# Kernel optimization log

Measured on AMD Instinct MI355X. Metric: run time of the kernel, lower is better.

## Reference

```python
import jax, jax.numpy as jnp
import numpy as np
import math

A, R, E, H = 4, 2, 12, 24  # msg_angular, msg_radial, embed_dim, hidden_dim
N = A * R
B, L = 131072, 15

def _ring_adj(n):
    adj = np.zeros((n, n), np.float32)
    if n == 1:
        adj[0, 0] = 1.0
    else:
        for i in range(n):
            adj[i, (i - 1) % n] = 1.0
            adj[i, (i + 1) % n] = 1.0
    return jnp.asarray(adj)

ANG_ADJ = _ring_adj(A)
RAD_ADJ = _ring_adj(R)

def setup_inputs():
    key = jax.random.key(0)
    ks = jax.random.split(key, 16)
    p = lambda k, s: jax.random.normal(k, s, jnp.float32) * 0.1
    return {
        "x": jax.random.normal(ks[0], (B, L, 4), jnp.float32),
        "enc_w1": p(ks[1], (4, H)), "enc_b1": p(ks[2], (H,)),
        "enc_w2": p(ks[3], (H, H)), "enc_b2": p(ks[4], (H,)),
        "enc_w3": p(ks[5], (H, 3)), "enc_b3": p(ks[6], (3,)),
        "node_w1": p(ks[7], (E, H)), "node_b1": p(ks[8], (H,)),
        "node_w2": p(ks[9], (H, E)), "node_b2": p(ks[10], (E,)),
        "angular_logit": jnp.zeros((A,), jnp.float32),
        "radial_logit": jnp.zeros((R,), jnp.float32),
        "read_w1": p(ks[11], (E * N, H)), "read_b1": p(ks[12], (H,)),
        "read_w2": p(ks[13], (H, 4)), "read_b2": p(ks[14], (4,)),
    }

def _norm_adj(logit, adj):
    a = jax.nn.softmax(logit)[None, :] * adj
    return a / jnp.maximum(a.sum(1, keepdims=True), 1e-6)

def _forward(x, enc_w1, enc_b1, enc_w2, enc_b2, enc_w3, enc_b3,
             node_w1, node_b1, node_w2, node_b2,
             angular_logit, radial_logit,
             read_w1, read_b1, read_w2, read_b2):
    b = x.shape[0]
    # encoder: original loops over all timesteps but only uses the last z
    zt = jnp.tanh(x[:, -1, :] @ enc_w1 + enc_b1)
    zt = jnp.tanh(zt @ enc_w2 + enc_b2)
    z = zt @ enc_w3 + enc_b3                       # [B, 3]
    r = jax.nn.sigmoid(z[:, 0]) * (R - 1)          # R_idx in [0, R-1]
    p = (z[:, 1] + math.pi) / (2 * math.pi) * A    # phi_idx (can be <0 or >A)
    # torch code calls .item(), detaching indices/weights from autograd
    r = jax.lax.stop_gradient(r)
    p = jax.lax.stop_gradient(p)
    r0 = jnp.trunc(r)   # int() truncates toward zero
    p0 = jnp.trunc(p)
    dr = (r - r0)[:, None]
    dp = (p - p0)[:, None]
    dro = jnp.array([0.0, 0.0, 1.0, 1.0], jnp.float32)   # 4 bilinear corners
    dpo = jnp.array([0.0, 1.0, 0.0, 1.0], jnp.float32)
    wr = jnp.where(dro == 0, 1.0 - dr, dr)               # [B, 4]
    wp = jnp.where(dpo == 0, 1.0 - dp, dp)
    w = wr * wp                                          # [B, 4]
    r_i = jnp.minimum(r0.astype(jnp.int32)[:, None] + dro.astype(jnp.int32), R - 1)
    p_i = jnp.mod(p0.astype(jnp.int32)[:, None] + dpo.astype(jnp.int32), A)
    mask = (w > 0).astype(x.dtype)[:, :, None]           # 'if weight > 0' skip
    # node_embed = pad(concat([z, weight]), E); z entries are NOT weight-scaled
    vec = jnp.concatenate([
        jnp.broadcast_to(z[:, None, :], (b, 4, 3)),
        w[:, :, None],
        jnp.zeros((b, 4, E - 4), x.dtype)], axis=-1) * mask   # [B, 4, E]
    grid = jnp.zeros((b, R, A, E), x.dtype).at[
        jnp.arange(b)[:, None], r_i, p_i].add(vec)            # scatter-add
    h = grid.reshape(b, N, E)
    ang = _norm_adj(angular_logit, ANG_ADJ)  # [A, A]
    rad = _norm_adj(radial_logit, RAD_ADJ)   # [R, R]
    # faithful to the torch .view() layout mixing (r,a,e)
    h_ang = jnp.einsum('ij,bjk->bik', ang, h.reshape(b, A, R * E)).reshape(b, N, E)
    h_rad = jnp.einsum('ij,bjk->bik', rad, h.reshape(b, R, A * E)).reshape(b, N, E)
    h = h + h_ang + h_rad
    h = jnp.tanh(h @ node_w1 + node_b1) @ node_w2 + node_b2   # node_net
    out = jnp.tanh(h.reshape(b, -1) @ read_w1 + read_b1) @ read_w2 + read_b2
    return out  # [B, 4]

def reference(x, enc_w1, enc_b1, enc_w2, enc_b2, enc_w3, enc_b3,
              node_w1, node_b1, node_w2, node_b2,
              angular_logit, radial_logit,
              read_w1, read_b1, read_w2, read_b2):
    return _forward(x, enc_w1, enc_b1, enc_w2, enc_b2, enc_w3, enc_b3,
                    node_w1, node_b1, node_w2, node_b2,
                    angular_logit, radial_logit,
                    read_w1, read_b1, read_w2, read_b2)
```

## Files before the change

kernel.cpp:

```cpp
#include <hip/hip_runtime.h>
#include <math.h>


#define PI_F 3.14159265358979323846f

typedef float f32x2 __attribute__((ext_vector_type(2)));

__device__ __forceinline__ f32x2 b2(float v) { f32x2 r; r.x = v; r.y = v; return r; }
__device__ __forceinline__ f32x2 pkfma(f32x2 a, f32x2 b, f32x2 c) {
    return __builtin_elementwise_fma(a, b, c);
}

__device__ __forceinline__ float fast_tanh(float v) {
    float e = __expf(2.0f * v);
    return 1.0f - 2.0f * __builtin_amdgcn_rcpf(e + 1.0f);
}

__device__ __forceinline__ f32x2 tanh2(f32x2 v) {
    f32x2 e; e.x = __expf(2.0f * v.x); e.y = __expf(2.0f * v.y);
    f32x2 ep = e + b2(1.0f);
    f32x2 r; r.x = __builtin_amdgcn_rcpf(ep.x); r.y = __builtin_amdgcn_rcpf(ep.y);
    return pkfma(b2(-2.0f), r, b2(1.0f));
}

__device__ __forceinline__ float quad_sum(float x) {
    x += __int_as_float(__builtin_amdgcn_update_dpp(
             0, __float_as_int(x), 0xB1, 0xF, 0xF, true));
    x += __int_as_float(__builtin_amdgcn_update_dpp(
             0, __float_as_int(x), 0x4E, 0xF, 0xF, true));
    return x;
}

__device__ __forceinline__ float xor4_sum(float x) {
    return x + __int_as_float(
        __builtin_amdgcn_ds_swizzle(__float_as_int(x), 0x101F));
}

#define K1_LDS 880

extern "C" __global__ void __launch_bounds__(256, 2)
topo_k1(const float* __restrict__ x,
        const float* __restrict__ ew1, const float* __restrict__ eb1,
        const float* __restrict__ ew2, const float* __restrict__ eb2,
        const float* __restrict__ ew3, const float* __restrict__ eb3,
        const float* __restrict__ alog, const float* __restrict__ rlog,
        const float* __restrict__ nw2, const float* __restrict__ nb2,
        const float* __restrict__ rw1, const float* __restrict__ rb1,
        float* __restrict__ ws, int B)
{
    const int nb1b = (B + 255) >> 8;

    if ((int)blockIdx.x >= nb1b) {
        const int gid = ((int)blockIdx.x - nb1b) * 256 + (int)threadIdx.x;
        float* M = ws + (size_t)B * 20;
        if (gid < 4608) {
            const int cell = gid / 576, rem = gid - cell * 576;
            const int j = rem / 24, j2 = rem - j * 24;
            double s = 0.0;
            #pragma unroll
            for (int d = 0; d < 12; ++d)
                s += (double)nw2[j * 12 + d] * (double)rw1[(cell * 12 + d) * 24 + j2];
            M[gid] = (float)s;
        } else if (gid < 4632) {
            const int j2 = gid - 4608;
            double s = (double)rb1[j2];
            for (int i = 0; i < 96; ++i)
                s += (double)nb2[i % 12] * (double)rw1[i * 24 + j2];
            M[4608 + j2] = (float)s;
        }
        return;
    }

    __shared__ float wf[K1_LDS];
    const float4* wq = reinterpret_cast<const float4*>(wf);
    {
        const int tt = threadIdx.x;
        for (int i = tt; i < 24; i += 256) {
            wf[i * 8 + 0] = ew1[i];
            wf[i * 8 + 1] = ew1[24 + i];
            wf[i * 8 + 2] = ew1[48 + i];
            wf[i * 8 + 3] = ew1[72 + i];
            wf[i * 8 + 4] = eb1[i];
        }
        for (int i = tt; i < 576; i += 256) wf[192 + i] = ew2[i];
        for (int i = tt; i < 24;  i += 256) wf[768 + i] = eb2[i];
        for (int i = tt; i < 72;  i += 256) wf[792 + (i % 3) * 24 + (i / 3)] = ew3[i];
        for (int i = tt; i < 3;   i += 256) wf[864 + i] = eb3[i];
    }
    __syncthreads();

    const int b = blockIdx.x * blockDim.x + threadIdx.x;
    if (b >= B) return;

    const float4 xv = *reinterpret_cast<const float4*>(x + (size_t)b * 60 + 56);

    f32x2 A2[12];
    #pragma unroll
    for (int c = 0; c < 6; ++c) {
        float4 b4 = wq[192 / 4 + c];
        A2[c*2+0].x = b4.x; A2[c*2+0].y = b4.y;
        A2[c*2+1].x = b4.z; A2[c*2+1].y = b4.w;
    }
    #pragma unroll 2
    for (int k = 0; k < 24; ++k) {
        float4 p  = wq[2 * k];
        float4 p2 = wq[2 * k + 1];
        const float zk = fast_tanh(p2.x + xv.x*p.x + xv.y*p.y + xv.z*p.z + xv.w*p.w);
        const f32x2 zk2 = b2(zk);
        const int rr = 48 + k * 6;
        #pragma unroll
        for (int c = 0; c < 6; ++c) {
            float4 rv = wq[rr + c];
            f32x2 r01; r01.x = rv.x; r01.y = rv.y;
            f32x2 r23; r23.x = rv.z; r23.y = rv.w;
            A2[c*2+0] = pkfma(zk2, r01, A2[c*2+0]);
            A2[c*2+1] = pkfma(zk2, r23, A2[c*2+1]);
        }
    }
    float zt2[24];
    #pragma unroll
    for (int j = 0; j < 24; ++j)
        zt2[j] = fast_tanh((j & 1) ? A2[j >> 1].y : A2[j >> 1].x);

    float z0 = wf[864], z1 = wf[865], z2 = wf[866];
    #pragma unroll
    for (int c = 0; c < 6; ++c) {
        float4 v0 = wq[198 + c], v1 = wq[204 + c], v2 = wq[210 + c];
        z0 += zt2[c*4+0]*v0.x + zt2[c*4+1]*v0.y + zt2[c*4+2]*v0.z + zt2[c*4+3]*v0.w;
        z1 += zt2[c*4+0]*v1.x + zt2[c*4+1]*v1.y + zt2[c*4+2]*v1.z + zt2[c*4+3]*v1.w;
        z2 += zt2[c*4+0]*v2.x + zt2[c*4+1]*v2.y + zt2[c*4+2]*v2.z + zt2[c*4+3]*v2.w;
    }

    float ang[4][4];
    {
        float m = fmaxf(fmaxf(alog[0], alog[1]), fmaxf(alog[2], alog[3]));
        float e0 = __expf(alog[0] - m), e1 = __expf(alog[1] - m);
        float e2 = __expf(alog[2] - m), e3 = __expf(alog[3] - m);
        float s = e0 + e1 + e2 + e3;
        float sm[4] = { e0 / s, e1 / s, e2 / s, e3 / s };
        #pragma unroll
        for (int i = 0; i < 4; ++i) {
            const int jn = (i + 3) & 3, jp = (i + 1) & 3;
            float inv = 1.0f / fmaxf(sm[jn] + sm[jp], 1e-6f);
            #pragma unroll
            for (int j = 0; j < 4; ++j) {
                float adj = (j == jn || j == jp) ? 1.0f : 0.0f;
                ang[i][j] = sm[j] * adj * inv;
            }
        }
    }
    float rad[2][2];
    {
        float m = fmaxf(rlog[0], rlog[1]);
        float f0 = __expf(rlog[0] - m), f1 = __expf(rlog[1] - m);
        float fs = f0 + f1;
        float sm0 = f0 / fs, sm1 = f1 / fs;
        rad[0][0] = 0.0f; rad[0][1] = sm1 / fmaxf(sm1, 1e-6f);
        rad[1][1] = 0.0f; rad[1][0] = sm0 / fmaxf(sm0, 1e-6f);
    }

    const float r = 1.0f / (1.0f + __expf(-z0));
    const float p = (z1 + PI_F) / (2.0f * PI_F) * 4.0f;
    const float r0f = truncf(r), p0f = truncf(p);
    const float dr = r - r0f, dp = p - p0f;
    const int r0i = (int)r0f, p0i = (int)p0f;

    const float w0c = (1.0f - dr) * (1.0f - dp);
    const float w1c = (1.0f - dr) * dp;
    const float w2c = dr * (1.0f - dp);
    const float w3c = dr * dp;

    const int ri0 = min(r0i, 1);
    const int ri2 = min(r0i + 1, 1);
    const int pi0 = p0i & 3;
    const int pi1 = (p0i + 1) & 3;

    const int c0 = ri0 * 4 + pi0, c1 = ri0 * 4 + pi1;
    const int c2 = ri2 * 4 + pi0, c3 = ri2 * 4 + pi1;

    float cnt[8], wsum[8];
    #pragma unroll
    for (int n = 0; n < 8; ++n) {
        float cm = 0.0f, cw = 0.0f;
        if (c0 == n && w0c > 0.0f) { cm += 1.0f; cw += w0c; }
        if (c1 == n && w1c > 0.0f) { cm += 1.0f; cw += w1c; }
        if (c2 == n && w2c > 0.0f) { cm += 1.0f; cw += w2c; }
        if (c3 == n && w3c > 0.0f) { cm += 1.0f; cw += w3c; }
        cnt[n] = cm; wsum[n] = cw;
    }
    float mc[8], mw[8];
    #pragma unroll
    for (int n = 0; n < 8; ++n) {
        float ac = cnt[n], aw = wsum[n];
        #pragma unroll
        for (int j = 0; j < 4; ++j) {
            const float g = ang[n >> 1][j];
            ac += g * cnt[2 * j + (n & 1)];
            aw += g * wsum[2 * j + (n & 1)];
        }
        #pragma unroll
        for (int j = 0; j < 2; ++j) {
            const float g = rad[n >> 2][j];
            ac += g * cnt[4 * j + (n & 3)];
            aw += g * wsum[4 * j + (n & 3)];
        }
        mc[n] = ac; mw[n] = aw;
    }

    float* wp = ws + (size_t)b * 20;
    float4 v0; v0.x = z0;    v0.y = z1;    v0.z = z2;    v0.w = 0.0f;
    float4 v1; v1.x = mc[0]; v1.y = mc[1]; v1.z = mc[2]; v1.w = mc[3];
    float4 v2; v2.x = mc[4]; v2.y = mc[5]; v2.z = mc[6]; v2.w = mc[7];
    float4 v3; v3.x = mw[0]; v3.y = mw[1]; v3.z = mw[2]; v3.w = mw[3];
    float4 v4; v4.x = mw[4]; v4.y = mw[5]; v4.z = mw[6]; v4.w = mw[7];
    reinterpret_cast<float4*>(wp)[0] = v0;
    reinterpret_cast<float4*>(wp)[1] = v1;
    reinterpret_cast<float4*>(wp)[2] = v2;
    reinterpret_cast<float4*>(wp)[3] = v3;
    reinterpret_cast<float4*>(wp)[4] = v4;
}

#define K2_LDS 4956

extern "C" __global__ void __launch_bounds__(256)
topo_k2(const float* __restrict__ ws,
        const float* __restrict__ nw1, const float* __restrict__ nb1,
        const float* __restrict__ rw2, const float* __restrict__ rb2,
        float* __restrict__ out, int B)
{
    __shared__ float wf[K2_LDS];
    const float4* wq = reinterpret_cast<const float4*>(wf);
    {
        const int tt = threadIdx.x;
        const float* Msrc = ws + (size_t)B * 20;
        for (int i = tt; i < 4608; i += 256) {
            const int cell = i / 576, rem = i - cell * 576;
            wf[192 + cell * 580 + rem] = Msrc[i];
        }
        for (int i = tt; i < 24; i += 256) wf[4832 + i] = Msrc[4608 + i];
        for (int i = tt; i < 24; i += 256) {
            wf[i * 8 + 0] = nw1[i];
            wf[i * 8 + 1] = nw1[24 + i];
            wf[i * 8 + 2] = nw1[48 + i];
            wf[i * 8 + 3] = nw1[72 + i];
            wf[i * 8 + 4] = nb1[i];
        }
        for (int i = tt; i < 96; i += 256) wf[4856 + i] = rw2[i];
        for (int i = tt; i < 4;  i += 256) wf[4952 + i] = rb2[i];
    }
    __syncthreads();

    const int tid  = blockIdx.x * blockDim.x + threadIdx.x;
    const int cp   = tid & 3;
    const int half = (tid >> 2) & 1;
    const int slot = tid >> 3;
    const int nP   = (B + 1) >> 1;
    if (slot >= nP) return;
    const int e0  = 2 * slot;
    const int e1s = 2 * slot + 1;
    const int e1  = (e1s < B) ? e1s : (B - 1);

    const float* wp0 = ws + (size_t)e0 * 20;
    const float* wp1 = ws + (size_t)e1 * 20;
    const float4 zA4 = *reinterpret_cast<const float4*>(wp0);
    const float4 zB4 = *reinterpret_cast<const float4*>(wp1);
    const float2 mc0 = *reinterpret_cast<const float2*>(wp0 + 4 + 2 * cp);
    const float2 mw0 = *reinterpret_cast<const float2*>(wp0 + 12 + 2 * cp);
    const float2 mc1 = *reinterpret_cast<const float2*>(wp1 + 4 + 2 * cp);
    const float2 mw1 = *reinterpret_cast<const float2*>(wp1 + 12 + 2 * cp);

    f32x2 ZX; ZX.x = zA4.x; ZX.y = zB4.x;
    f32x2 ZY; ZY.x = zA4.y; ZY.y = zB4.y;
    f32x2 ZZ; ZZ.x = zA4.z; ZZ.y = zB4.z;
    f32x2 MCA; MCA.x = mc0.x; MCA.y = mc1.x;
    f32x2 MCB; MCB.x = mc0.y; MCB.y = mc1.y;
    f32x2 MWA; MWA.x = mw0.x; MWA.y = mw1.x;
    f32x2 MWB; MWB.x = mw0.y; MWB.y = mw1.y;

    const int mA = 48 + (2 * cp) * 145 + half * 3;
    const int mB = mA + 145;

    f32x2 T0[6], T1[6];
    #pragma unroll
    for (int k = 0; k < 6; ++k) { T0[k] = b2(0.0f); T1[k] = b2(0.0f); }

    #pragma unroll 1
    for (int j = 0; j < 24; ++j) {
        float4 pk  = wq[2 * j];
        float4 pk2 = wq[2 * j + 1];
        f32x2 Q = ZX * b2(pk.x);
        Q = pkfma(ZY, b2(pk.y), Q);
        Q = pkfma(ZZ, b2(pk.z), Q);
        f32x2 baseA = pkfma(MWA, b2(pk.w), b2(pk2.x));
        f32x2 baseB = pkfma(MWB, b2(pk.w), b2(pk2.x));
        f32x2 HA = tanh2(pkfma(MCA, Q, baseA));
        f32x2 HB = tanh2(pkfma(MCB, Q, baseB));

        const int ra = mA + j * 6, rb = mB + j * 6;
        float4 a0 = wq[ra], a1 = wq[ra + 1], a2v = wq[ra + 2];
        float4 bb0 = wq[rb], bb1 = wq[rb + 1], bb2 = wq[rb + 2];
        f32x2 A0; A0.x = a0.x;  A0.y = a0.y;
        f32x2 A1; A1.x = a0.z;  A1.y = a0.w;
        f32x2 A2; A2.x = a1.x;  A2.y = a1.y;
        f32x2 A3; A3.x = a1.z;  A3.y = a1.w;
        f32x2 A4; A4.x = a2v.x; A4.y = a2v.y;
        f32x2 A5; A5.x = a2v.z; A5.y = a2v.w;
        f32x2 B0; B0.x = bb0.x; B0.y = bb0.y;
        f32x2 B1; B1.x = bb0.z; B1.y = bb0.w;
        f32x2 B2; B2.x = bb1.x; B2.y = bb1.y;
        f32x2 B3; B3.x = bb1.z; B3.y = bb1.w;
        f32x2 B4; B4.x = bb2.x; B4.y = bb2.y;
        f32x2 B5; B5.x = bb2.z; B5.y = bb2.w;

        const f32x2 hA0 = b2(HA.x), hA1 = b2(HA.y);
        const f32x2 hB0 = b2(HB.x), hB1 = b2(HB.y);
        T0[0] = pkfma(hA0, A0, T0[0]); T0[1] = pkfma(hA0, A1, T0[1]);
        T0[2] = pkfma(hA0, A2, T0[2]); T0[3] = pkfma(hA0, A3, T0[3]);
        T0[4] = pkfma(hA0, A4, T0[4]); T0[5] = pkfma(hA0, A5, T0[5]);
        T1[0] = pkfma(hA1, A0, T1[0]); T1[1] = pkfma(hA1, A1, T1[1]);
        T1[2] = pkfma(hA1, A2, T1[2]); T1[3] = pkfma(hA1, A3, T1[3]);
        T1[4] = pkfma(hA1, A4, T1[4]); T1[5] = pkfma(hA1, A5, T1[5]);
        T0[0] = pkfma(hB0, B0, T0[0]); T0[1] = pkfma(hB0, B1, T0[1]);
        T0[2] = pkfma(hB0, B2, T0[2]); T0[3] = pkfma(hB0, B3, T0[3]);
        T0[4] = pkfma(hB0, B4, T0[4]); T0[5] = pkfma(hB0, B5, T0[5]);
        T1[0] = pkfma(hB1, B0, T1[0]); T1[1] = pkfma(hB1, B1, T1[1]);
        T1[2] = pkfma(hB1, B2, T1[2]); T1[3] = pkfma(hB1, B3, T1[3]);
        T1[4] = pkfma(hB1, B4, T1[4]); T1[5] = pkfma(hB1, B5, T1[5]);
    }

    float t0[12], t1[12];
    #pragma unroll
    for (int k = 0; k < 12; ++k) {
        t0[k] = (k & 1) ? T0[k >> 1].y : T0[k >> 1].x;
        t1[k] = (k & 1) ? T1[k >> 1].y : T1[k >> 1].x;
    }

    #pragma unroll
    for (int k = 0; k < 12; ++k) {
        t0[k] = quad_sum(t0[k]);
        t1[k] = quad_sum(t1[k]);
    }
    #pragma unroll
    for (int c = 0; c < 3; ++c) {
        float4 ti = wq[1208 + half * 3 + c];
        t0[c*4+0] += ti.x; t0[c*4+1] += ti.y; t0[c*4+2] += ti.z; t0[c*4+3] += ti.w;
        t1[c*4+0] += ti.x; t1[c*4+1] += ti.y; t1[c*4+2] += ti.z; t1[c*4+3] += ti.w;
    }

    float o00 = 0.0f, o01 = 0.0f, o02 = 0.0f, o03 = 0.0f;
    float o10 = 0.0f, o11 = 0.0f, o12 = 0.0f, o13 = 0.0f;
    #pragma unroll
    for (int k = 0; k < 12; ++k) {
        const float tv0 = fast_tanh(t0[k]);
        const float tv1 = fast_tanh(t1[k]);
        float4 rv = wq[1214 + half * 12 + k];
        o00 += tv0 * rv.x; o01 += tv0 * rv.y; o02 += tv0 * rv.z; o03 += tv0 * rv.w;
        o10 += tv1 * rv.x; o11 += tv1 * rv.y; o12 += tv1 * rv.z; o13 += tv1 * rv.w;
    }
    o00 = xor4_sum(o00); o01 = xor4_sum(o01); o02 = xor4_sum(o02); o03 = xor4_sum(o03);
    o10 = xor4_sum(o10); o11 = xor4_sum(o11); o12 = xor4_sum(o12); o13 = xor4_sum(o13);

    if ((tid & 7) == 0) {
        float4 ob = wq[1238];
        float4 ovA; ovA.x = o00 + ob.x; ovA.y = o01 + ob.y;
        ovA.z = o02 + ob.z; ovA.w = o03 + ob.w;
        *reinterpret_cast<float4*>(out + (size_t)e0 * 4) = ovA;
        if (e1s < B) {
            float4 ovB; ovB.x = o10 + ob.x; ovB.y = o11 + ob.y;
            ovB.z = o12 + ob.z; ovB.w = o13 + ob.w;
            *reinterpret_cast<float4*>(out + (size_t)e1s * 4) = ovB;
        }
    }
}

extern "C" __global__ void __launch_bounds__(256, 2)
topo_fused(const float* __restrict__ x,
           const float* __restrict__ ew1, const float* __restrict__ eb1,
           const float* __restrict__ ew2, const float* __restrict__ eb2,
           const float* __restrict__ ew3, const float* __restrict__ eb3,
           const float* __restrict__ nw1, const float* __restrict__ nb1,
           const float* __restrict__ nw2, const float* __restrict__ nb2,
           const float* __restrict__ alog, const float* __restrict__ rlog,
           const float* __restrict__ rw1, const float* __restrict__ rb1,
           const float* __restrict__ rw2, const float* __restrict__ rb2,
           float* __restrict__ out, int B)
{
    const int b = blockIdx.x * blockDim.x + threadIdx.x;
    if (b >= B) return;

    float ang[4][4];
    {
        float m = fmaxf(fmaxf(alog[0], alog[1]), fmaxf(alog[2], alog[3]));
        float e0 = __expf(alog[0] - m), e1 = __expf(alog[1] - m);
        float e2 = __expf(alog[2] - m), e3 = __expf(alog[3] - m);
        float s = e0 + e1 + e2 + e3;
        float sm[4] = { e0 / s, e1 / s, e2 / s, e3 / s };
        #pragma unroll
        for (int i = 0; i < 4; ++i) {
            const int jn = (i + 3) & 3, jp = (i + 1) & 3;
            float inv = 1.0f / fmaxf(sm[jn] + sm[jp], 1e-6f);
            #pragma unroll
            for (int j = 0; j < 4; ++j) {
                float adj = (j == jn || j == jp) ? 1.0f : 0.0f;
                ang[i][j] = sm[j] * adj * inv;
            }
        }
    }
    float rad[2][2];
    {
        float m = fmaxf(rlog[0], rlog[1]);
        float f0 = __expf(rlog[0] - m), f1 = __expf(rlog[1] - m);
        float fs = f0 + f1;
        float sm0 = f0 / fs, sm1 = f1 / fs;
        rad[0][0] = 0.0f; rad[0][1] = sm1 / fmaxf(sm1, 1e-6f);
        rad[1][1] = 0.0f; rad[1][0] = sm0 / fmaxf(sm0, 1e-6f);
    }

    const float4 xv = *reinterpret_cast<const float4*>(x + (size_t)b * 60 + 56);
    float zt[24];
    #pragma unroll
    for (int j = 0; j < 24; ++j) {
        float a = eb1[j];
        a += xv.x * ew1[j];
        a += xv.y * ew1[24 + j];
        a += xv.z * ew1[48 + j];
        a += xv.w * ew1[72 + j];
        zt[j] = fast_tanh(a);
    }
    float z0 = eb3[0], z1 = eb3[1], z2 = eb3[2];
    #pragma unroll
    for (int j = 0; j < 24; ++j) {
        float a = eb2[j];
        #pragma unroll
        for (int k = 0; k < 24; ++k) a += zt[k] * ew2[k * 24 + j];
        const float z2t = fast_tanh(a);
        z0 += z2t * ew3[j * 3 + 0];
        z1 += z2t * ew3[j * 3 + 1];
        z2 += z2t * ew3[j * 3 + 2];
    }

    const float r = 1.0f / (1.0f + __expf(-z0));
    const float p = (z1 + PI_F) / (2.0f * PI_F) * 4.0f;
    const float r0f = truncf(r), p0f = truncf(p);
    const float dr = r - r0f, dp = p - p0f;
    const int r0i = (int)r0f, p0i = (int)p0f;
    const float w0c = (1.0f - dr) * (1.0f - dp);
    const float w1c = (1.0f - dr) * dp;
    const float w2c = dr * (1.0f - dp);
    const float w3c = dr * dp;
    const int ri0 = min(r0i, 1);
    const int ri2 = min(r0i + 1, 1);
    const int pi0 = p0i & 3;
    const int pi1 = (p0i + 1) & 3;
    const int c0 = ri0 * 4 + pi0, c1 = ri0 * 4 + pi1;
    const int c2 = ri2 * 4 + pi0, c3 = ri2 * 4 + pi1;

    float cnt[8], wsum[8];
    #pragma unroll
    for (int n = 0; n < 8; ++n) {
        float cm = 0.0f, cw = 0.0f;
        if (c0 == n && w0c > 0.0f) { cm += 1.0f; cw += w0c; }
        if (c1 == n && w1c > 0.0f) { cm += 1.0f; cw += w1c; }
        if (c2 == n && w2c > 0.0f) { cm += 1.0f; cw += w2c; }
        if (c3 == n && w3c > 0.0f) { cm += 1.0f; cw += w3c; }
        cnt[n] = cm; wsum[n] = cw;
    }
    float mc[8], mw[8];
    #pragma unroll
    for (int n = 0; n < 8; ++n) {
        float ac = cnt[n], aw = wsum[n];
        #pragma unroll
        for (int j = 0; j < 4; ++j) {
            const float g = ang[n >> 1][j];
            ac += g * cnt[2 * j + (n & 1)];
            aw += g * wsum[2 * j + (n & 1)];
        }
        #pragma unroll
        for (int j = 0; j < 2; ++j) {
            const float g = rad[n >> 2][j];
            ac += g * cnt[4 * j + (n & 3)];
            aw += g * wsum[4 * j + (n & 3)];
        }
        mc[n] = ac; mw[n] = aw;
    }

    float t[24];
    #pragma unroll
    for (int j = 0; j < 24; ++j) t[j] = rb1[j];
    #pragma unroll
    for (int n = 0; n < 8; ++n) {
        const float f0 = mc[n] * z0, f1 = mc[n] * z1, f2 = mc[n] * z2;
        float ho[12];
        #pragma unroll
        for (int d = 0; d < 12; ++d) ho[d] = nb2[d];
        #pragma unroll
        for (int j = 0; j < 24; ++j) {
            const float hj = fast_tanh(nb1[j] + f0 * nw1[j] + f1 * nw1[24 + j]
                                       + f2 * nw1[48 + j] + mw[n] * nw1[72 + j]);
            #pragma unroll
            for (int d = 0; d < 12; ++d) ho[d] += hj * nw2[j * 12 + d];
        }
        #pragma unroll
        for (int d = 0; d < 12; ++d) {
            const int rbase = (n * 12 + d) * 24;
            #pragma unroll
            for (int j2 = 0; j2 < 24; ++j2) t[j2] += ho[d] * rw1[rbase + j2];
        }
    }

    float o0 = rb2[0], o1 = rb2[1], o2 = rb2[2], o3 = rb2[3];
    #pragma unroll
    for (int j = 0; j < 24; ++j) {
        const float tt = fast_tanh(t[j]);
        o0 += tt * rw2[j * 4 + 0];
        o1 += tt * rw2[j * 4 + 1];
        o2 += tt * rw2[j * 4 + 2];
        o3 += tt * rw2[j * 4 + 3];
    }
    float4 ov; ov.x = o0; ov.y = o1; ov.z = o2; ov.w = o3;
    *reinterpret_cast<float4*>(out + (size_t)b * 4) = ov;
}

extern "C" void kernel_launch(void* const* d_in, const int* in_sizes, int n_in,
                              void* d_out, int out_size, void* d_ws, size_t ws_size,
                              hipStream_t stream) {
    const float* x    = (const float*)d_in[0];
    const float* ew1  = (const float*)d_in[1];
    const float* eb1  = (const float*)d_in[2];
    const float* ew2  = (const float*)d_in[3];
    const float* eb2  = (const float*)d_in[4];
    const float* ew3  = (const float*)d_in[5];
    const float* eb3  = (const float*)d_in[6];
    const float* nw1  = (const float*)d_in[7];
    const float* nb1  = (const float*)d_in[8];
    const float* nw2  = (const float*)d_in[9];
    const float* nb2  = (const float*)d_in[10];
    const float* alog = (const float*)d_in[11];
    const float* rlog = (const float*)d_in[12];
    const float* rw1  = (const float*)d_in[13];
    const float* rb1  = (const float*)d_in[14];
    const float* rw2  = (const float*)d_in[15];
    const float* rb2  = (const float*)d_in[16];
    float* out = (float*)d_out;

    const int B = in_sizes[0] / 60;
    const size_t ws_needed = ((size_t)B * 20 + 4632) * sizeof(float);

    if (ws_size >= ws_needed) {
        float* ws = (float*)d_ws;
        const int nb1b = (B + 255) / 256;
        const int g1 = nb1b + 19;
        topo_k1<<<g1, 256, 0, stream>>>(x, ew1, eb1, ew2, eb2, ew3, eb3,
                                        alog, rlog, nw2, nb2, rw1, rb1, ws, B);
        const long long nP = ((long long)B + 1) / 2;
        const long long tot2 = nP * 8;
        const int g2 = (int)((tot2 + 255) / 256);
        topo_k2<<<g2, 256, 0, stream>>>(ws, nw1, nb1, rw2, rb2, out, B);
    } else {
        const int g = (B + 255) / 256;
        topo_fused<<<g, 256, 0, stream>>>(
            x, ew1, eb1, ew2, eb2, ew3, eb3, nw1, nb1, nw2, nb2,
            alog, rlog, rw1, rb1, rw2, rb2, out, B);
    }
}
```

Baseline: 50.21 us.

## Fuse encoder and readout kernels into one block-per-64-samples kernel

Replaces the two-kernel pipeline, which passed per-sample features through a global workspace, with one fused kernel. Each block handles 64 samples: half the threads run the encoder with two threads per sample (pair reduction through DPP), while the other half compute the folded node_w2·read_w1 matrix into LDS. The readout stage then runs from LDS in the same block. This removes the workspace round trip and one kernel launch, but every block now recomputes the 4632-entry folded weight matrix in float instead of double, adding redundant per-block work and using more LDS.

```diff
diff --git a/kernel.cpp b/kernel.cpp
--- a/kernel.cpp
+++ b/kernel.cpp
@@ -7,6 +7,7 @@
 typedef float f32x2 __attribute__((ext_vector_type(2)));
 
 __device__ __forceinline__ f32x2 b2(float v) { f32x2 r; r.x = v; r.y = v; return r; }
+__device__ __forceinline__ f32x2 mk2(float a, float b) { f32x2 r; r.x = a; r.y = b; return r; }
 __device__ __forceinline__ f32x2 pkfma(f32x2 a, f32x2 b, f32x2 c) {
     return __builtin_elementwise_fma(a, b, c);
 }
@@ -21,6 +22,12 @@
     f32x2 ep = e + b2(1.0f);
     f32x2 r; r.x = __builtin_amdgcn_rcpf(ep.x); r.y = __builtin_amdgcn_rcpf(ep.y);
     return pkfma(b2(-2.0f), r, b2(1.0f));
+}
+
+__device__ __forceinline__ float pair_sum(float x) {
+    x += __int_as_float(__builtin_amdgcn_update_dpp(
+             0, __float_as_int(x), 0xB1, 0xF, 0xF, true));
+    return x;
 }
 
 __device__ __forceinline__ float quad_sum(float x) {
@@ -36,45 +43,25 @@
         __builtin_amdgcn_ds_swizzle(__float_as_int(x), 0x101F));
 }
 
-#define K1_LDS 880
+#define FUSED_LDS 7116
 
 extern "C" __global__ void __launch_bounds__(256, 2)
-topo_k1(const float* __restrict__ x,
-        const float* __restrict__ ew1, const float* __restrict__ eb1,
-        const float* __restrict__ ew2, const float* __restrict__ eb2,
-        const float* __restrict__ ew3, const float* __restrict__ eb3,
-        const float* __restrict__ alog, const float* __restrict__ rlog,
-        const float* __restrict__ nw2, const float* __restrict__ nb2,
-        const float* __restrict__ rw1, const float* __restrict__ rb1,
-        float* __restrict__ ws, int B)
+topo_fused64(const float* __restrict__ x,
+             const float* __restrict__ ew1, const float* __restrict__ eb1,
+             const float* __restrict__ ew2, const float* __restrict__ eb2,
+             const float* __restrict__ ew3, const float* __restrict__ eb3,
+             const float* __restrict__ nw1, const float* __restrict__ nb1,
+             const float* __restrict__ nw2, const float* __restrict__ nb2,
+             const float* __restrict__ alog, const float* __restrict__ rlog,
+             const float* __restrict__ rw1, const float* __restrict__ rb1,
+             const float* __restrict__ rw2, const float* __restrict__ rb2,
+             float* __restrict__ out, int B)
 {
-    const int nb1b = (B + 255) >> 8;
-
-    if ((int)blockIdx.x >= nb1b) {
-        const int gid = ((int)blockIdx.x - nb1b) * 256 + (int)threadIdx.x;
-        float* M = ws + (size_t)B * 20;
-        if (gid < 4608) {
-            const int cell = gid / 576, rem = gid - cell * 576;
-            const int j = rem / 24, j2 = rem - j * 24;
-            double s = 0.0;
-            #pragma unroll
-            for (int d = 0; d < 12; ++d)
-                s += (double)nw2[j * 12 + d] * (double)rw1[(cell * 12 + d) * 24 + j2];
-            M[gid] = (float)s;
-        } else if (gid < 4632) {
-            const int j2 = gid - 4608;
-            double s = (double)rb1[j2];
-            for (int i = 0; i < 96; ++i)
-                s += (double)nb2[i % 12] * (double)rw1[i * 24 + j2];
-            M[4608 + j2] = (float)s;
-        }
-        return;
-    }
-
-    __shared__ float wf[K1_LDS];
+    __shared__ float wf[FUSED_LDS];
     const float4* wq = reinterpret_cast<const float4*>(wf);
+    const int tt = threadIdx.x;
+
     {
-        const int tt = threadIdx.x;
         for (int i = tt; i < 24; i += 256) {
             wf[i * 8 + 0] = ew1[i];
             wf[i * 8 + 1] = ew1[24 + i];
@@ -86,198 +73,196 @@
         for (int i = tt; i < 24;  i += 256) wf[768 + i] = eb2[i];
         for (int i = tt; i < 72;  i += 256) wf[792 + (i % 3) * 24 + (i / 3)] = ew3[i];
         for (int i = tt; i < 3;   i += 256) wf[864 + i] = eb3[i];
+        for (int i = tt; i < 24;  i += 256) {
+            wf[880 + i * 8 + 0] = nw1[i];
+            wf[880 + i * 8 + 1] = nw1[24 + i];
+            wf[880 + i * 8 + 2] = nw1[48 + i];
+            wf[880 + i * 8 + 3] = nw1[72 + i];
+            wf[880 + i * 8 + 4] = nb1[i];
+        }
+        for (int i = tt; i < 96; i += 256) wf[5736 + i] = rw2[i];
+        for (int i = tt; i < 4;  i += 256) wf[5832 + i] = rb2[i];
     }
     __syncthreads();
 
-    const int b = blockIdx.x * blockDim.x + threadIdx.x;
-    if (b >= B) return;
-
-    const float4 xv = *reinterpret_cast<const float4*>(x + (size_t)b * 60 + 56);
-
-    f32x2 A2[12];
-    #pragma unroll
-    for (int c = 0; c < 6; ++c) {
-        float4 b4 = wq[192 / 4 + c];
-        A2[c*2+0].x = b4.x; A2[c*2+0].y = b4.y;
-        A2[c*2+1].x = b4.z; A2[c*2+1].y = b4.w;
-    }
-    #pragma unroll 2
-    for (int k = 0; k < 24; ++k) {
-        float4 p  = wq[2 * k];
-        float4 p2 = wq[2 * k + 1];
-        const float zk = fast_tanh(p2.x + xv.x*p.x + xv.y*p.y + xv.z*p.z + xv.w*p.w);
-        const f32x2 zk2 = b2(zk);
-        const int rr = 48 + k * 6;
-        #pragma unroll
-        for (int c = 0; c < 6; ++c) {
-            float4 rv = wq[rr + c];
-            f32x2 r01; r01.x = rv.x; r01.y = rv.y;
-            f32x2 r23; r23.x = rv.z; r23.y = rv.w;
-            A2[c*2+0] = pkfma(zk2, r01, A2[c*2+0]);
-            A2[c*2+1] = pkfma(zk2, r23, A2[c*2+1]);
-        }
-    }
-    float zt2[24];
-    #pragma unroll
-    for (int j = 0; j < 24; ++j)
-        zt2[j] = fast_tanh((j & 1) ? A2[j >> 1].y : A2[j >> 1].x);
-
-    float z0 = wf[864], z1 = wf[865], z2 = wf[866];
-    #pragma unroll
-    for (int c = 0; c < 6; ++c) {
-        float4 v0 = wq[198 + c], v1 = wq[204 + c], v2 = wq[210 + c];
-        z0 += zt2[c*4+0]*v0.x + zt2[c*4+1]*v0.y + zt2[c*4+2]*v0.z + zt2[c*4+3]*v0.w;
-        z1 += zt2[c*4+0]*v1.x + zt2[c*4+1]*v1.y + zt2[c*4+2]*v1.z + zt2[c*4+3]*v1.w;
-        z2 += zt2[c*4+0]*v2.x + zt2[c*4+1]*v2.y + zt2[c*4+2]*v2.z + zt2[c*4+3]*v2.w;
-    }
-
-    float ang[4][4];
-    {
-        float m = fmaxf(fmaxf(alog[0], alog[1]), fmaxf(alog[2], alog[3]));
-        float e0 = __expf(alog[0] - m), e1 = __expf(alog[1] - m);
-        float e2 = __expf(alog[2] - m), e3 = __expf(alog[3] - m);
-        float s = e0 + e1 + e2 + e3;
-        float sm[4] = { e0 / s, e1 / s, e2 / s, e3 / s };
-        #pragma unroll
-        for (int i = 0; i < 4; ++i) {
-            const int jn = (i + 3) & 3, jp = (i + 1) & 3;
-            float inv = 1.0f / fmaxf(sm[jn] + sm[jp], 1e-6f);
+    const int base = blockIdx.x * 64;
+
+    if (tt < 128) {
+        const int el = tt >> 1;
+        const int h  = tt & 1;
+        const int b  = base + el;
+
+        const float4 xv = *reinterpret_cast<const float4*>(x + (size_t)b * 60 + 56);
+
+        float a2h[12];
+        #pragma unroll
+        for (int c = 0; c < 3; ++c) {
+            float4 b4 = wq[192 + 3 * h + c];
+            a2h[c*4+0] = b4.x; a2h[c*4+1] = b4.y;
+            a2h[c*4+2] = b4.z; a2h[c*4+3] = b4.w;
+        }
+        #pragma unroll 2
+        for (int k = 0; k < 24; ++k) {
+            float4 p  = wq[2 * k];
+            float4 p2 = wq[2 * k + 1];
+            const float zk = fast_tanh(p2.x + xv.x*p.x + xv.y*p.y + xv.z*p.z + xv.w*p.w);
+            #pragma unroll
+            for (int c = 0; c < 3; ++c) {
+                float4 rv = wq[48 + 6 * k + 3 * h + c];
+                a2h[c*4+0] += zk * rv.x; a2h[c*4+1] += zk * rv.y;
+                a2h[c*4+2] += zk * rv.z; a2h[c*4+3] += zk * rv.w;
+            }
+        }
+        float zt2h[12];
+        #pragma unroll
+        for (int j = 0; j < 12; ++j) zt2h[j] = fast_tanh(a2h[j]);
+
+        float z0p = 0.0f, z1p = 0.0f, z2p = 0.0f;
+        #pragma unroll
+        for (int c = 0; c < 3; ++c) {
+            float4 v0 = wq[198 + 3 * h + c];
+            float4 v1 = wq[204 + 3 * h + c];
+            float4 v2 = wq[210 + 3 * h + c];
+            z0p += zt2h[c*4+0]*v0.x + zt2h[c*4+1]*v0.y + zt2h[c*4+2]*v0.z + zt2h[c*4+3]*v0.w;
+            z1p += zt2h[c*4+0]*v1.x + zt2h[c*4+1]*v1.y + zt2h[c*4+2]*v1.z + zt2h[c*4+3]*v1.w;
+            z2p += zt2h[c*4+0]*v2.x + zt2h[c*4+1]*v2.y + zt2h[c*4+2]*v2.z + zt2h[c*4+3]*v2.w;
+        }
+        const float z0 = pair_sum(z0p) + wf[864];
+        const float z1 = pair_sum(z1p) + wf[865];
+        const float z2 = pair_sum(z2p) + wf[866];
+
+        float ang[4][4];
+        {
+            float m = fmaxf(fmaxf(alog[0], alog[1]), fmaxf(alog[2], alog[3]));
+            float e0 = __expf(alog[0] - m), e1 = __expf(alog[1] - m);
+            float e2 = __expf(alog[2] - m), e3 = __expf(alog[3] - m);
+            float s = e0 + e1 + e2 + e3;
+            float sm[4] = { e0 / s, e1 / s, e2 / s, e3 / s };
+            #pragma unroll
+            for (int i = 0; i < 4; ++i) {
+                const int jn = (i + 3) & 3, jp = (i + 1) & 3;
+                float inv = 1.0f / fmaxf(sm[jn] + sm[jp], 1e-6f);
+                #pragma unroll
+                for (int j = 0; j < 4; ++j) {
+                    float adj = (j == jn || j == jp) ? 1.0f : 0.0f;
+                    ang[i][j] = sm[j] * adj * inv;
+                }
+            }
+        }
+        float rad[2][2];
+        {
+            float m = fmaxf(rlog[0], rlog[1]);
+            float f0 = __expf(rlog[0] - m), f1 = __expf(rlog[1] - m);
+            float fs = f0 + f1;
+            float sm0 = f0 / fs, sm1 = f1 / fs;
+            rad[0][0] = 0.0f; rad[0][1] = sm1 / fmaxf(sm1, 1e-6f);
+            rad[1][1] = 0.0f; rad[1][0] = sm0 / fmaxf(sm0, 1e-6f);
+        }
+
+        const float r = 1.0f / (1.0f + __expf(-z0));
+        const float p = (z1 + PI_F) / (2.0f * PI_F) * 4.0f;
+        const float r0f = truncf(r), p0f = truncf(p);
+        const float dr = r - r0f, dp = p - p0f;
+        const int r0i = (int)r0f, p0i = (int)p0f;
+
+        const float w0c = (1.0f - dr) * (1.0f - dp);
+        const float w1c = (1.0f - dr) * dp;
+        const float w2c = dr * (1.0f - dp);
+        const float w3c = dr * dp;
+
+        const int ri0 = min(r0i, 1);
+        const int ri2 = min(r0i + 1, 1);
+        const int pi0 = p0i & 3;
+        const int pi1 = (p0i + 1) & 3;
+
+        const int c0 = ri0 * 4 + pi0, c1 = ri0 * 4 + pi1;
+        const int c2 = ri2 * 4 + pi0, c3 = ri2 * 4 + pi1;
+
+        float cnt[8], wsum[8];
+        #pragma unroll
+        for (int n = 0; n < 8; ++n) {
+            float cm = 0.0f, cw = 0.0f;
+            if (c0 == n && w0c > 0.0f) { cm += 1.0f; cw += w0c; }
+            if (c1 == n && w1c > 0.0f) { cm += 1.0f; cw += w1c; }
+            if (c2 == n && w2c > 0.0f) { cm += 1.0f; cw += w2c; }
+            if (c3 == n && w3c > 0.0f) { cm += 1.0f; cw += w3c; }
+            cnt[n] = cm; wsum[n] = cw;
+        }
+        float mc[8], mw[8];
+        #pragma unroll
+        for (int n = 0; n < 8; ++n) {
+            float ac = cnt[n], aw = wsum[n];
             #pragma unroll
             for (int j = 0; j < 4; ++j) {
-                float adj = (j == jn || j == jp) ? 1.0f : 0.0f;
-                ang[i][j] = sm[j] * adj * inv;
+                const float g = ang[n >> 1][j];
+                ac += g * cnt[2 * j + (n & 1)];
+                aw += g * wsum[2 * j + (n & 1)];
             }
-        }
-    }
-    float rad[2][2];
-    {
-        float m = fmaxf(rlog[0], rlog[1]);
-        float f0 = __expf(rlog[0] - m), f1 = __expf(rlog[1] - m);
-        float fs = f0 + f1;
-        float sm0 = f0 / fs, sm1 = f1 / fs;
-        rad[0][0] = 0.0f; rad[0][1] = sm1 / fmaxf(sm1, 1e-6f);
-        rad[1][1] = 0.0f; rad[1][0] = sm0 / fmaxf(sm0, 1e-6f);
-    }
-
-    const float r = 1.0f / (1.0f + __expf(-z0));
-    const float p = (z1 + PI_F) / (2.0f * PI_F) * 4.0f;
-    const float r0f = truncf(r), p0f = truncf(p);
-    const float dr = r - r0f, dp = p - p0f;
-    const int r0i = (int)r0f, p0i = (int)p0f;
-
-    const float w0c = (1.0f - dr) * (1.0f - dp);
-    const float w1c = (1.0f - dr) * dp;
-    const float w2c = dr * (1.0f - dp);
-    const float w3c = dr * dp;
-
-    const int ri0 = min(r0i, 1);
-    const int ri2 = min(r0i + 1, 1);
-    const int pi0 = p0i & 3;
-    const int pi1 = (p0i + 1) & 3;
-
-    const int c0 = ri0 * 4 + pi0, c1 = ri0 * 4 + pi1;
-    const int c2 = ri2 * 4 + pi0, c3 = ri2 * 4 + pi1;
-
-    float cnt[8], wsum[8];
-    #pragma unroll
-    for (int n = 0; n < 8; ++n) {
-        float cm = 0.0f, cw = 0.0f;
-        if (c0 == n && w0c > 0.0f) { cm += 1.0f; cw += w0c; }
-        if (c1 == n && w1c > 0.0f) { cm += 1.0f; cw += w1c; }
-        if (c2 == n && w2c > 0.0f) { cm += 1.0f; cw += w2c; }
-        if (c3 == n && w3c > 0.0f) { cm += 1.0f; cw += w3c; }
-        cnt[n] = cm; wsum[n] = cw;
-    }
-    float mc[8], mw[8];
-    #pragma unroll
-    for (int n = 0; n < 8; ++n) {
-        float ac = cnt[n], aw = wsum[n];
-        #pragma unroll
-        for (int j = 0; j < 4; ++j) {
-            const float g = ang[n >> 1][j];
-            ac += g * cnt[2 * j + (n & 1)];
-            aw += g * wsum[2 * j + (n & 1)];
-        }
-        #pragma unroll
-        for (int j = 0; j < 2; ++j) {
-            const float g = rad[n >> 2][j];
-            ac += g * cnt[4 * j + (n & 3)];
-            aw += g * wsum[4 * j + (n & 3)];
-        }
-        mc[n] = ac; mw[n] = aw;
-    }
-
-    float* wp = ws + (size_t)b * 20;
-    float4 v0; v0.x = z0;    v0.y = z1;    v0.z = z2;    v0.w = 0.0f;
-    float4 v1; v1.x = mc[0]; v1.y = mc[1]; v1.z = mc[2]; v1.w = mc[3];
-    float4 v2; v2.x = mc[4]; v2.y = mc[5]; v2.z = mc[6]; v2.w = mc[7];
-    float4 v3; v3.x = mw[0]; v3.y = mw[1]; v3.z = mw[2]; v3.w = mw[3];
-    float4 v4; v4.x = mw[4]; v4.y = mw[5]; v4.z = mw[6]; v4.w = mw[7];
-    reinterpret_cast<float4*>(wp)[0] = v0;
-    reinterpret_cast<float4*>(wp)[1] = v1;
-    reinterpret_cast<float4*>(wp)[2] = v2;
-    reinterpret_cast<float4*>(wp)[3] = v3;
-    reinterpret_cast<float4*>(wp)[4] = v4;
-}
-
-#define K2_LDS 4956
-
-extern "C" __global__ void __launch_bounds__(256)
-topo_k2(const float* __restrict__ ws,
-        const float* __restrict__ nw1, const float* __restrict__ nb1,
-        const float* __restrict__ rw2, const float* __restrict__ rb2,
-        float* __restrict__ out, int B)
-{
-    __shared__ float wf[K2_LDS];
-    const float4* wq = reinterpret_cast<const float4*>(wf);
-    {
-        const int tt = threadIdx.x;
-        const float* Msrc = ws + (size_t)B * 20;
-        for (int i = tt; i < 4608; i += 256) {
+            #pragma unroll
+            for (int j = 0; j < 2; ++j) {
+                const float g = rad[n >> 2][j];
+                ac += g * cnt[4 * j + (n & 3)];
+                aw += g * wsum[4 * j + (n & 3)];
+            }
+            mc[n] = ac; mw[n] = aw;
+        }
+
+        if (h == 0) {
+            float4* sp = reinterpret_cast<float4*>(&wf[5836 + 20 * el]);
+            float4 v0; v0.x = z0;    v0.y = z1;    v0.z = z2;    v0.w = 0.0f;
+            float4 v1; v1.x = mc[0]; v1.y = mc[1]; v1.z = mc[2]; v1.w = mc[3];
+            float4 v2; v2.x = mc[4]; v2.y = mc[5]; v2.z = mc[6]; v2.w = mc[7];
+            float4 v3; v3.x = mw[0]; v3.y = mw[1]; v3.z = mw[2]; v3.w = mw[3];
+            float4 v4; v4.x = mw[4]; v4.y = mw[5]; v4.z = mw[6]; v4.w = mw[7];
+            sp[0] = v0; sp[1] = v1; sp[2] = v2; sp[3] = v3; sp[4] = v4;
+        }
+    } else {
+        const int w = tt - 128;
+        #pragma unroll 1
+        for (int t = 0; t < 36; ++t) {
+            const int i = w + 128 * t;
             const int cell = i / 576, rem = i - cell * 576;
-            wf[192 + cell * 580 + rem] = Msrc[i];
-        }
-        for (int i = tt; i < 24; i += 256) wf[4832 + i] = Msrc[4608 + i];
-        for (int i = tt; i < 24; i += 256) {
-            wf[i * 8 + 0] = nw1[i];
-            wf[i * 8 + 1] = nw1[24 + i];
-            wf[i * 8 + 2] = nw1[48 + i];
-            wf[i * 8 + 3] = nw1[72 + i];
-            wf[i * 8 + 4] = nb1[i];
-        }
-        for (int i = tt; i < 96; i += 256) wf[4856 + i] = rw2[i];
-        for (int i = tt; i < 4;  i += 256) wf[4952 + i] = rb2[i];
+            const int j = rem / 24, j2 = rem - j * 24;
+            float s = 0.0f;
+            #pragma unroll
+            for (int d = 0; d < 12; ++d)
+                s += nw2[j * 12 + d] * rw1[(cell * 12 + d) * 24 + j2];
+            wf[1072 + cell * 580 + rem] = s;
+        }
+        if (w < 24) {
+            float s = rb1[w];
+            #pragma unroll 1
+            for (int i = 0; i < 96; ++i)
+                s += nb2[i % 12] * rw1[i * 24 + w];
+            wf[5712 + w] = s;
+        }
     }
     __syncthreads();
 
-    const int tid  = blockIdx.x * blockDim.x + threadIdx.x;
-    const int cp   = tid & 3;
-    const int half = (tid >> 2) & 1;
-    const int slot = tid >> 3;
-    const int nP   = (B + 1) >> 1;
-    if (slot >= nP) return;
-    const int e0  = 2 * slot;
-    const int e1s = 2 * slot + 1;
-    const int e1  = (e1s < B) ? e1s : (B - 1);
-
-    const float* wp0 = ws + (size_t)e0 * 20;
-    const float* wp1 = ws + (size_t)e1 * 20;
-    const float4 zA4 = *reinterpret_cast<const float4*>(wp0);
-    const float4 zB4 = *reinterpret_cast<const float4*>(wp1);
-    const float2 mc0 = *reinterpret_cast<const float2*>(wp0 + 4 + 2 * cp);
-    const float2 mw0 = *reinterpret_cast<const float2*>(wp0 + 12 + 2 * cp);
-    const float2 mc1 = *reinterpret_cast<const float2*>(wp1 + 4 + 2 * cp);
-    const float2 mw1 = *reinterpret_cast<const float2*>(wp1 + 12 + 2 * cp);
-
-    f32x2 ZX; ZX.x = zA4.x; ZX.y = zB4.x;
-    f32x2 ZY; ZY.x = zA4.y; ZY.y = zB4.y;
-    f32x2 ZZ; ZZ.x = zA4.z; ZZ.y = zB4.z;
-    f32x2 MCA; MCA.x = mc0.x; MCA.y = mc1.x;
-    f32x2 MCB; MCB.x = mc0.y; MCB.y = mc1.y;
-    f32x2 MWA; MWA.x = mw0.x; MWA.y = mw1.x;
-    f32x2 MWB; MWB.x = mw0.y; MWB.y = mw1.y;
-
-    const int mA = 48 + (2 * cp) * 145 + half * 3;
+    const int cp   = tt & 3;
+    const int half = (tt >> 2) & 1;
+    const int slot = tt >> 3;
+    const int eL0  = 2 * slot;
+    const int eL1  = 2 * slot + 1;
+
+    const float* sp0 = &wf[5836 + 20 * eL0];
+    const float* sp1 = &wf[5836 + 20 * eL1];
+    const float4 zA4 = *reinterpret_cast<const float4*>(sp0);
+    const float4 zB4 = *reinterpret_cast<const float4*>(sp1);
+    const float2 mc0 = *reinterpret_cast<const float2*>(sp0 + 4 + 2 * cp);
+    const float2 mw0 = *reinterpret_cast<const float2*>(sp0 + 12 + 2 * cp);
+    const float2 mc1 = *reinterpret_cast<const float2*>(sp1 + 4 + 2 * cp);
+    const float2 mw1 = *reinterpret_cast<const float2*>(sp1 + 12 + 2 * cp);
+
+    const f32x2 ZX = mk2(zA4.x, zB4.x);
+    const f32x2 ZY = mk2(zA4.y, zB4.y);
+    const f32x2 ZZ = mk2(zA4.z, zB4.z);
+    const f32x2 MCA = mk2(mc0.x, mc1.x);
+    const f32x2 MCB = mk2(mc0.y, mc1.y);
+    const f32x2 MWA = mk2(mw0.x, mw1.x);
+    const f32x2 MWB = mk2(mw0.y, mw1.y);
+
+    const int mA = 268 + (2 * cp) * 145 + half * 3;
     const int mB = mA + 145;
 
     f32x2 T0[6], T1[6];
@@ -286,8 +271,8 @@
 
     #pragma unroll 1
     for (int j = 0; j < 24; ++j) {
-        float4 pk  = wq[2 * j];
-        float4 pk2 = wq[2 * j + 1];
+        float4 pk  = wq[220 + 2 * j];
+        float4 pk2 = wq[220 + 2 * j + 1];
         f32x2 Q = ZX * b2(pk.x);
         Q = pkfma(ZY, b2(pk.y), Q);
         Q = pkfma(ZZ, b2(pk.z), Q);
@@ -299,50 +284,37 @@
         const int ra = mA + j * 6, rb = mB + j * 6;
         float4 a0 = wq[ra], a1 = wq[ra + 1], a2v = wq[ra + 2];
         float4 bb0 = wq[rb], bb1 = wq[rb + 1], bb2 = wq[rb + 2];
-        f32x2 A0; A0.x = a0.x;  A0.y = a0.y;
-        f32x2 A1; A1.x = a0.z;  A1.y = a0.w;
-        f32x2 A2; A2.x = a1.x;  A2.y = a1.y;
-        f32x2 A3; A3.x = a1.z;  A3.y = a1.w;
-        f32x2 A4; A4.x = a2v.x; A4.y = a2v.y;
-        f32x2 A5; A5.x = a2v.z; A5.y = a2v.w;
-        f32x2 B0; B0.x = bb0.x; B0.y = bb0.y;
-        f32x2 B1; B1.x = bb0.z; B1.y = bb0.w;
-        f32x2 B2; B2.x = bb1.x; B2.y = bb1.y;
-        f32x2 B3; B3.x = bb1.z; B3.y = bb1.w;
-        f32x2 B4; B4.x = bb2.x; B4.y = bb2.y;
-        f32x2 B5; B5.x = bb2.z; B5.y = bb2.w;
-
-        const f32x2 hA0 = b2(HA.x), hA1 = b2(HA.y);
-        const f32x2 hB0 = b2(HB.x), hB1 = b2(HB.y);
-        T0[0] = pkfma(hA0, A0, T0[0]); T0[1] = pkfma(hA0, A1, T0[1]);
-        T0[2] = pkfma(hA0, A2, T0[2]); T0[3] = pkfma(hA0, A3, T0[3]);
-        T0[4] = pkfma(hA0, A4, T0[4]); T0[5] = pkfma(hA0, A5, T0[5]);
-        T1[0] = pkfma(hA1, A0, T1[0]); T1[1] = pkfma(hA1, A1, T1[1]);
-        T1[2] = pkfma(hA1, A2, T1[2]); T1[3] = pkfma(hA1, A3, T1[3]);
-        T1[4] = pkfma(hA1, A4, T1[4]); T1[5] = pkfma(hA1, A5, T1[5]);
-        T0[0] = pkfma(hB0, B0, T0[0]); T0[1] = pkfma(hB0, B1, T0[1]);
-        T0[2] = pkfma(hB0, B2, T0[2]); T0[3] = pkfma(hB0, B3, T0[3]);
-        T0[4] = pkfma(hB0, B4, T0[4]); T0[5] = pkfma(hB0, B5, T0[5]);
-        T1[0] = pkfma(hB1, B0, T1[0]); T1[1] = pkfma(hB1, B1, T1[1]);
-        T1[2] = pkfma(hB1, B2, T1[2]); T1[3] = pkfma(hB1, B3, T1[3]);
-        T1[4] = pkfma(hB1, B4, T1[4]); T1[5] = pkfma(hB1, B5, T1[5]);
+        const f32x2 A0 = mk2(a0.x, a0.y),   A1 = mk2(a0.z, a0.w);
+        const f32x2 A2 = mk2(a1.x, a1.y),   A3 = mk2(a1.z, a1.w);
+        const f32x2 A4 = mk2(a2v.x, a2v.y), A5 = mk2(a2v.z, a2v.w);
+        const f32x2 B0 = mk2(bb0.x, bb0.y), B1 = mk2(bb0.z, bb0.w);
+        const f32x2 B2 = mk2(bb1.x, bb1.y), B3 = mk2(bb1.z, bb1.w);
+        const f32x2 B4 = mk2(bb2.x, bb2.y), B5 = mk2(bb2.z, bb2.w);
+
+        f32x2 h;
+        h = b2(HA.x);
+        T0[0]=pkfma(h,A0,T0[0]); T0[1]=pkfma(h,A1,T0[1]); T0[2]=pkfma(h,A2,T0[2]);
+        T0[3]=pkfma(h,A3,T0[3]); T0[4]=pkfma(h,A4,T0[4]); T0[5]=pkfma(h,A5,T0[5]);
+        h = b2(HB.x);
+        T0[0]=pkfma(h,B0,T0[0]); T0[1]=pkfma(h,B1,T0[1]); T0[2]=pkfma(h,B2,T0[2]);
+        T0[3]=pkfma(h,B3,T0[3]); T0[4]=pkfma(h,B4,T0[4]); T0[5]=pkfma(h,B5,T0[5]);
+        h = b2(HA.y);
+        T1[0]=pkfma(h,A0,T1[0]); T1[1]=pkfma(h,A1,T1[1]); T1[2]=pkfma(h,A2,T1[2]);
+        T1[3]=pkfma(h,A3,T1[3]); T1[4]=pkfma(h,A4,T1[4]); T1[5]=pkfma(h,A5,T1[5]);
+        h = b2(HB.y);
+        T1[0]=pkfma(h,B0,T1[0]); T1[1]=pkfma(h,B1,T1[1]); T1[2]=pkfma(h,B2,T1[2]);
+        T1[3]=pkfma(h,B3,T1[3]); T1[4]=pkfma(h,B4,T1[4]); T1[5]=pkfma(h,B5,T1[5]);
     }
 
     float t0[12], t1[12];
     #pragma unroll
     for (int k = 0; k < 12; ++k) {
-        t0[k] = (k & 1) ? T0[k >> 1].y : T0[k >> 1].x;
-        t1[k] = (k & 1) ? T1[k >> 1].y : T1[k >> 1].x;
-    }
-
-    #pragma unroll
-    for (int k = 0; k < 12; ++k) {
-        t0[k] = quad_sum(t0[k]);
-        t1[k] = quad_sum(t1[k]);
+        t0[k] = quad_sum((k & 1) ? T0[k >> 1].y : T0[k >> 1].x);
+        t1[k] = quad_sum((k & 1) ? T1[k >> 1].y : T1[k >> 1].x);
     }
     #pragma unroll
     for (int c = 0; c < 3; ++c) {
-        float4 ti = wq[1208 + half * 3 + c];
+        float4 ti = wq[1428 + half * 3 + c];
         t0[c*4+0] += ti.x; t0[c*4+1] += ti.y; t0[c*4+2] += ti.z; t0[c*4+3] += ti.w;
         t1[c*4+0] += ti.x; t1[c*4+1] += ti.y; t1[c*4+2] += ti.z; t1[c*4+3] += ti.w;
     }
@@ -353,37 +325,36 @@
     for (int k = 0; k < 12; ++k) {
         const float tv0 = fast_tanh(t0[k]);
         const float tv1 = fast_tanh(t1[k]);
-        float4 rv = wq[1214 + half * 12 + k];
+        float4 rv = wq[1434 + half * 12 + k];
         o00 += tv0 * rv.x; o01 += tv0 * rv.y; o02 += tv0 * rv.z; o03 += tv0 * rv.w;
         o10 += tv1 * rv.x; o11 += tv1 * rv.y; o12 += tv1 * rv.z; o13 += tv1 * rv.w;
     }
     o00 = xor4_sum(o00); o01 = xor4_sum(o01); o02 = xor4_sum(o02); o03 = xor4_sum(o03);
     o10 = xor4_sum(o10); o11 = xor4_sum(o11); o12 = xor4_sum(o12); o13 = xor4_sum(o13);
 
-    if ((tid & 7) == 0) {
-        float4 ob = wq[1238];
+    if ((tt & 7) == 0) {
+        float4 ob = wq[1458];
+        const int e0g = base + eL0;
         float4 ovA; ovA.x = o00 + ob.x; ovA.y = o01 + ob.y;
         ovA.z = o02 + ob.z; ovA.w = o03 + ob.w;
-        *reinterpret_cast<float4*>(out + (size_t)e0 * 4) = ovA;
-        if (e1s < B) {
-            float4 ovB; ovB.x = o10 + ob.x; ovB.y = o11 + ob.y;
-            ovB.z = o12 + ob.z; ovB.w = o13 + ob.w;
-            *reinterpret_cast<float4*>(out + (size_t)e1s * 4) = ovB;
-        }
+        *reinterpret_cast<float4*>(out + (size_t)e0g * 4) = ovA;
+        float4 ovB; ovB.x = o10 + ob.x; ovB.y = o11 + ob.y;
+        ovB.z = o12 + ob.z; ovB.w = o13 + ob.w;
+        *reinterpret_cast<float4*>(out + (size_t)(e0g + 1) * 4) = ovB;
     }
 }
 
 extern "C" __global__ void __launch_bounds__(256, 2)
-topo_fused(const float* __restrict__ x,
-           const float* __restrict__ ew1, const float* __restrict__ eb1,
-           const float* __restrict__ ew2, const float* __restrict__ eb2,
-           const float* __restrict__ ew3, const float* __restrict__ eb3,
-           const float* __restrict__ nw1, const float* __restrict__ nb1,
-           const float* __restrict__ nw2, const float* __restrict__ nb2,
-           const float* __restrict__ alog, const float* __restrict__ rlog,
-           const float* __restrict__ rw1, const float* __restrict__ rb1,
-           const float* __restrict__ rw2, const float* __restrict__ rb2,
-           float* __restrict__ out, int B)
+topo_fb(const float* __restrict__ x,
+        const float* __restrict__ ew1, const float* __restrict__ eb1,
+        const float* __restrict__ ew2, const float* __restrict__ eb2,
+        const float* __restrict__ ew3, const float* __restrict__ eb3,
+        const float* __restrict__ nw1, const float* __restrict__ nb1,
+        const float* __restrict__ nw2, const float* __restrict__ nb2,
+        const float* __restrict__ alog, const float* __restrict__ rlog,
+        const float* __restrict__ rw1, const float* __restrict__ rb1,
+        const float* __restrict__ rw2, const float* __restrict__ rb2,
+        float* __restrict__ out, int B)
 {
     const int b = blockIdx.x * blockDim.x + threadIdx.x;
     if (b >= B) return;
@@ -511,11 +482,11 @@
     float o0 = rb2[0], o1 = rb2[1], o2 = rb2[2], o3 = rb2[3];
     #pragma unroll
     for (int j = 0; j < 24; ++j) {
-        const float tt = fast_tanh(t[j]);
-        o0 += tt * rw2[j * 4 + 0];
-        o1 += tt * rw2[j * 4 + 1];
-        o2 += tt * rw2[j * 4 + 2];
-        o3 += tt * rw2[j * 4 + 3];
+        const float tt2 = fast_tanh(t[j]);
+        o0 += tt2 * rw2[j * 4 + 0];
+        o1 += tt2 * rw2[j * 4 + 1];
+        o2 += tt2 * rw2[j * 4 + 2];
+        o3 += tt2 * rw2[j * 4 + 3];
     }
     float4 ov; ov.x = o0; ov.y = o1; ov.z = o2; ov.w = o3;
     *reinterpret_cast<float4*>(out + (size_t)b * 4) = ov;
@@ -544,21 +515,15 @@
     float* out = (float*)d_out;
 
     const int B = in_sizes[0] / 60;
-    const size_t ws_needed = ((size_t)B * 20 + 4632) * sizeof(float);
-
-    if (ws_size >= ws_needed) {
-        float* ws = (float*)d_ws;
-        const int nb1b = (B + 255) / 256;
-        const int g1 = nb1b + 19;
-        topo_k1<<<g1, 256, 0, stream>>>(x, ew1, eb1, ew2, eb2, ew3, eb3,
-                                        alog, rlog, nw2, nb2, rw1, rb1, ws, B);
-        const long long nP = ((long long)B + 1) / 2;
-        const long long tot2 = nP * 8;
-        const int g2 = (int)((tot2 + 255) / 256);
-        topo_k2<<<g2, 256, 0, stream>>>(ws, nw1, nb1, rw2, rb2, out, B);
+
+    if (B % 64 == 0) {
+        const int grid = B / 64;
+        topo_fused64<<<grid, 256, 0, stream>>>(
+            x, ew1, eb1, ew2, eb2, ew3, eb3, nw1, nb1, nw2, nb2,
+            alog, rlog, rw1, rb1, rw2, rb2, out, B);
     } else {
         const int g = (B + 255) / 256;
-        topo_fused<<<g, 256, 0, stream>>>(
+        topo_fb<<<g, 256, 0, stream>>>(
             x, ew1, eb1, ew2, eb2, ew3, eb3, nw1, nb1, nw2, nb2,
             alog, rlog, rw1, rb1, rw2, rb2, out, B);
     }
```

Result: slower. 67.72 us (+34.9%).
